# Kernel tuning notes

Hardware: AMD Instinct MI355X
Metric: run time of the kernel (lower is better)

The kernel has to match this reference:

```python
import jax, jax.numpy as jnp
import numpy as np

H = 1024      # hidden_dim == memory_dim (required by seq-axis concat)
M = 1024      # memory_dim
FF = 4096     # ff_dim
WIN = 16      # window_size
SLOTS = 10    # persistent memory slots
B, S = 2, 4096
EPS_LN = 1e-5
EPS_NORM = 1e-12


def _layernorm(x, g, b):
    m = jnp.mean(x, axis=-1, keepdims=True)
    v = jnp.var(x, axis=-1, keepdims=True)
    return (x - m) / jnp.sqrt(v + EPS_LN) * g + b


def setup_inputs() -> dict:
    key = jax.random.key(0)
    ks = jax.random.split(key, 12)

    def lin_w(k, out_d, in_d):
        return jax.random.normal(k, (out_d, in_d), jnp.float32) / np.sqrt(in_d)

    return {
        "x": jax.random.normal(ks[0], (B, S, H), jnp.float32),
        "mem_W": lin_w(ks[1], M, M), "mem_b": jnp.zeros((M,), jnp.float32),
        "P": jax.random.normal(ks[2], (SLOTS, M), jnp.float32),
        "Wi": lin_w(ks[3], M, H), "bi": jnp.zeros((M,), jnp.float32),
        "Wl1": lin_w(ks[4], M, M), "bl1": jnp.zeros((M,), jnp.float32),
        "Wl2": lin_w(ks[5], M, M), "bl2": jnp.zeros((M,), jnp.float32),
        "Wo": lin_w(ks[6], H, M), "bo": jnp.zeros((H,), jnp.float32),
        "fgate": jnp.ones((1,), jnp.float32),
        "lrate": jnp.ones((1,), jnp.float32),
        "Wg": lin_w(ks[7], H, 2 * H), "bg": jnp.zeros((H,), jnp.float32),
        "W1": lin_w(ks[8], FF, H), "b1": jnp.zeros((FF,), jnp.float32),
        "W2": lin_w(ks[9], H, FF), "b2": jnp.zeros((H,), jnp.float32),
        "g1": jnp.ones((H,), jnp.float32), "be1": jnp.zeros((H,), jnp.float32),
        "g2": jnp.ones((H,), jnp.float32), "be2": jnp.zeros((H,), jnp.float32),
        "g3": jnp.ones((H,), jnp.float32), "be3": jnp.zeros((H,), jnp.float32),
    }


def reference(x, mem_W, mem_b, P, Wi, bi, Wl1, bl1, Wl2, bl2, Wo, bo,
              fgate, lrate, Wg, bg, W1, b1, W2, b2,
              g1, be1, g2, be2, g3, be3):
    b, s, h = x.shape
    # k = concat(x, persistent) along seq; v = k.clone()
    k_full = jnp.concatenate([x, jnp.broadcast_to(P, (b,) + P.shape)], axis=1)  # [B, S+SLOTS, H]

    # sit at positions >= S and are never inside the window, so only x is attended.
    idx = jnp.arange(s)[:, None] + jnp.arange(-WIN, 1)[None, :]
    valid = idx >= 0
    k_win = k_full[:, jnp.maximum(idx, 0)]
    scores = jnp.einsum('bsh,bswh->bsw', x, k_win) * (h ** -0.5)
    scores = jnp.where(valid[None], scores, -jnp.inf)
    attn_out = jnp.einsum('bsw,bswh->bsh', jax.nn.softmax(scores, axis=-1), k_win)
    x1 = _layernorm(x + attn_out, g1, be1)

    # --- neural long-term memory (key == value since v = k.clone())
    kv = k_full.reshape(-1, h)
    kn = kv / jnp.maximum(jnp.linalg.norm(kv, axis=-1, keepdims=True), EPS_NORM)
    kp = kn @ Wi.T + bi          # projected key; value_proj is identical
    vp = kp
    hdd = jax.nn.silu(kp @ Wl1.T + bl1)
    hdd = jax.nn.silu(hdd @ Wl2.T + bl2)
    pred = hdd @ mem_W.T + mem_b
    diff = pred - vp
    n, m = diff.shape
    grad_W = (2.0 / (n * m)) * diff.T @ hdd          # d mse / d mem_W
    W_new = (1.0 - fgate) * mem_W + lrate * grad_W   # test-time memory update
    mem_out = hdd @ W_new.T + mem_b
    mo = (mem_out @ Wo.T + bo).reshape(b, -1, h)[:, :s]  # align with x seq length

    # --- gated fusion + FFN
    gate = jax.nn.sigmoid(jnp.concatenate([x1, mo], axis=-1) @ Wg.T + bg)
    combined = gate * x1 + (1.0 - gate) * mo
    x2 = _layernorm(x1 + combined, g2, be2)
    ff = jax.nn.silu(x2 @ W1.T + b1) @ W2.T + b2
    return _layernorm(x2 + ff, g3, be3)
```

## Files before the change

kernel.cpp:

```cpp
#include <hip/hip_runtime.h>
#include <hip/hip_bf16.h>

#define WIN 16
#define SLOTS 10
#define SS 4096
#define NTOK 8192
#define NKV 8212
#define NPOS 4106

typedef unsigned short u16;
typedef unsigned int u32;
typedef __attribute__((ext_vector_type(8))) short short8;
typedef __attribute__((ext_vector_type(4))) float f32x4;

__device__ __forceinline__ u16 f2bf(float f){
  union { float f; u32 u; } a; a.f = f;
  u32 r = (a.u + 0x7fff + ((a.u >> 16) & 1)) >> 16;
  return (u16)r;
}
__device__ __forceinline__ float bf2f(u16 v){
  union { u32 u; float f; } a; a.u = ((u32)v) << 16;
  return a.f;
}

#define GLOAD(gp, lp) __builtin_amdgcn_global_load_lds( \
    (const __attribute__((address_space(1))) void*)(gp), \
    (__attribute__((address_space(3))) void*)(lp), 16, 0, 0)

#define FENCE_BARRIER() do { \
    __builtin_amdgcn_sched_barrier(0); \
    __builtin_amdgcn_s_barrier(); \
    __builtin_amdgcn_sched_barrier(0); \
  } while(0)

__global__ __launch_bounds__(256) void cvt_bf16(const float4* __restrict__ in,
                                                ushort4* __restrict__ out, int n4){
  int i = blockIdx.x * 256 + threadIdx.x;
  if (i < n4){
    float4 v = in[i];
    ushort4 o; o.x=f2bf(v.x); o.y=f2bf(v.y); o.z=f2bf(v.z); o.w=f2bf(v.w);
    out[i] = o;
  }
}

__global__ __launch_bounds__(256) void attn_ln1(
    const float* __restrict__ x, const float* __restrict__ g1,
    const float* __restrict__ be1, u16* __restrict__ x1b)
{
  const int n = blockIdx.x;
  const int b = n >> 12, s = n & 4095;
  const int t = threadIdx.x, lane = t & 63, w = t >> 6;
  const float* xb = x + ((size_t)b << 22);
  const float4 q = ((const float4*)(xb + ((size_t)s << 10)))[t];
  const int j0 = (s >= WIN) ? 0 : (WIN - s);
  float kvv[17][4];
  float part[17];
  #pragma unroll
  for (int j=0;j<17;j++){
    float4 kk = make_float4(0.f,0.f,0.f,0.f);
    if (j >= j0) kk = ((const float4*)(xb + ((size_t)(s - WIN + j) << 10)))[t];
    kvv[j][0]=kk.x; kvv[j][1]=kk.y; kvv[j][2]=kk.z; kvv[j][3]=kk.w;
    part[j] = q.x*kk.x + q.y*kk.y + q.z*kk.z + q.w*kk.w;
  }
  __shared__ float red[17][4];
  #pragma unroll
  for (int j=0;j<17;j++){
    float v = part[j];
    #pragma unroll
    for (int off=32; off; off>>=1) v += __shfl_xor(v, off, 64);
    if (lane == 0) red[j][w] = v;
  }
  __syncthreads();
  __shared__ float wsh[17];
  if (t == 0){
    float sc[17];
    float mx = -3.0e38f;
    #pragma unroll
    for (int j=0;j<17;j++){
      float v = (red[j][0]+red[j][1]+red[j][2]+red[j][3]) * 0.03125f;
      sc[j] = v;
      if (j >= j0) mx = fmaxf(mx, v);
    }
    float ssum = 0.f;
    #pragma unroll
    for (int j=0;j<17;j++){
      float e = (j >= j0) ? expf(sc[j]-mx) : 0.f;
      wsh[j] = e; ssum += e;
    }
    float inv = 1.f/ssum;
    #pragma unroll
    for (int j=0;j<17;j++) wsh[j] *= inv;
  }
  __syncthreads();
  float y0=q.x, y1=q.y, y2=q.z, y3=q.w;
  #pragma unroll
  for (int j=0;j<17;j++){
    float wj = wsh[j];
    y0 += wj*kvv[j][0]; y1 += wj*kvv[j][1]; y2 += wj*kvv[j][2]; y3 += wj*kvv[j][3];
  }
  float s1 = y0+y1+y2+y3;
  float s2 = y0*y0+y1*y1+y2*y2+y3*y3;
  #pragma unroll
  for (int off=32; off; off>>=1){ s1 += __shfl_xor(s1, off, 64); s2 += __shfl_xor(s2, off, 64); }
  __shared__ float rsh[8];
  if (lane == 0){ rsh[w] = s1; rsh[4+w] = s2; }
  __syncthreads();
  float S1 = rsh[0]+rsh[1]+rsh[2]+rsh[3];
  float S2 = rsh[4]+rsh[5]+rsh[6]+rsh[7];
  float mean = S1 * (1.f/1024.f);
  float var  = S2 * (1.f/1024.f) - mean*mean;
  float rstd = 1.f/sqrtf(var + 1e-5f);
  float4 gv = ((const float4*)g1)[t];
  float4 bv = ((const float4*)be1)[t];
  ushort4 ob;
  ob.x = f2bf((y0-mean)*rstd*gv.x + bv.x);
  ob.y = f2bf((y1-mean)*rstd*gv.y + bv.y);
  ob.z = f2bf((y2-mean)*rstd*gv.z + bv.z);
  ob.w = f2bf((y3-mean)*rstd*gv.w + bv.w);
  ((ushort4*)x1b)[((size_t)n << 8) + t] = ob;
}

__global__ __launch_bounds__(256) void kv_norm(const float* __restrict__ x,
                                               const float* __restrict__ P,
                                               u16* __restrict__ kn)
{
  const int r = blockIdx.x;
  const int t = threadIdx.x, lane = t & 63, w = t >> 6;
  const int b = r / NPOS;
  const int pos = r - b*NPOS;
  const float* src = (pos < SS) ? (x + (((size_t)b*SS + pos) << 10))
                                : (P + ((size_t)(pos - SS) << 10));
  float4 v = ((const float4*)src)[t];
  float s2 = v.x*v.x + v.y*v.y + v.z*v.z + v.w*v.w;
  #pragma unroll
  for (int off=32; off; off>>=1) s2 += __shfl_xor(s2, off, 64);
  __shared__ float sh[4];
  if (lane == 0) sh[w] = s2;
  __syncthreads();
  float S = sh[0]+sh[1]+sh[2]+sh[3];
  float inv = 1.f / fmaxf(sqrtf(S), 1e-12f);
  ushort4 o; o.x=f2bf(v.x*inv); o.y=f2bf(v.y*inv); o.z=f2bf(v.z*inv); o.w=f2bf(v.w*inv);
  ((ushort4*)kn)[((size_t)r << 8) + t] = o;
}

template<int EPI, int SPLITA>
__global__ __launch_bounds__(256) void gemm_nt(
    const u16* __restrict__ A, const u16* __restrict__ A2,
    const u16* __restrict__ Bmat, const float* __restrict__ bias,
    const u16* __restrict__ auxb,
    float* __restrict__ Cf, u16* __restrict__ Cb,
    int N, int O, int ldA, int ldB, int klen)
{
  __shared__ __align__(16) u16 lA[2][128*64];
  __shared__ __align__(16) u16 lB[2][128*64];
  const int t = threadIdx.x;
  const int lane = t & 63;
  const int bm0 = blockIdx.x * 128;
  const int bn0 = blockIdx.y * 128;
  const int wid = t >> 6;
  const int wr = wid >> 1, wc = wid & 1;
  const int nkt = klen >> 6;

  f32x4 acc[4][4];
  #pragma unroll
  for (int i=0;i<4;i++)
    #pragma unroll
    for (int j=0;j<4;j++)
      acc[i][j] = (f32x4){0.f,0.f,0.f,0.f};

  const int srow = t >> 3;
  const int schunk = (((t & 7) ^ (srow & 7)) << 3);

  const u16* baseA[4]; const u16* baseA2[4]; const u16* baseB[4];
  #pragma unroll
  for (int i=0;i<4;i++){
    int gr = bm0 + srow + i*32; gr = gr < N ? gr : N-1;
    baseA[i] = A + (size_t)gr*(size_t)ldA + schunk;
    if (SPLITA) baseA2[i] = A2 + ((size_t)gr << 10) + schunk;
    int gb = bn0 + srow + i*32; gb = gb < O ? gb : O-1;
    baseB[i] = Bmat + (size_t)gb*(size_t)ldB + schunk;
  }

  auto stage = [&](int kt, int buf){
    const int kb = kt << 6;
    #pragma unroll
    for (int i=0;i<4;i++){
      const u16* src = SPLITA ? ((kb < 1024) ? baseA[i] + kb : baseA2[i] + (kb - 1024))
                              : baseA[i] + kb;
      GLOAD(src, &lA[buf][(i*256 + t) << 3]);
    }
    #pragma unroll
    for (int i=0;i<4;i++)
      GLOAD(baseB[i] + kb, &lB[buf][(i*256 + t) << 3]);
  };

  stage(0, 0);
  if (nkt > 1) stage(1, 1);

  const int l15 = lane & 15;
  const int rx = l15 & 7;
  const int cq = lane >> 4;

  for (int kt = 0; kt < nkt; ++kt){
    const int cur = kt & 1;
    if (kt + 1 < nkt) { asm volatile("s_waitcnt vmcnt(8)" ::: "memory"); }
    else              { asm volatile("s_waitcnt vmcnt(0)" ::: "memory"); }
    FENCE_BARRIER();
    #pragma unroll
    for (int kk=0;kk<2;kk++){
      const int soff = (((kk*4 + cq) ^ rx) << 3);
      short8 af[4], bfv[4];
      #pragma unroll
      for (int mi=0;mi<4;mi++)
        af[mi] = *(const short8*)(&lA[cur][((wr*64 + mi*16 + l15) << 6) + soff]);
      #pragma unroll
      for (int ni=0;ni<4;ni++)
        bfv[ni] = *(const short8*)(&lB[cur][((wc*64 + ni*16 + l15) << 6) + soff]);
      #pragma unroll
      for (int mi=0;mi<4;mi++)
        #pragma unroll
        for (int ni=0;ni<4;ni++)
          acc[mi][ni] = __builtin_amdgcn_mfma_f32_16x16x32_bf16(af[mi], bfv[ni], acc[mi][ni], 0, 0, 0);
    }
    FENCE_BARRIER();
    if (kt + 2 < nkt) stage(kt + 2, cur);
  }

  const int rbase = (lane >> 4) * 4;
  const int cidx = lane & 15;
  #pragma unroll
  for (int mi=0;mi<4;mi++){
    #pragma unroll
    for (int r=0;r<4;r++){
      const int n = bm0 + wr*64 + mi*16 + rbase + r;
      if (n >= N) continue;
      #pragma unroll
      for (int ni=0;ni<4;ni++){
        const int o = bn0 + wc*64 + ni*16 + cidx;
        float v = acc[mi][ni][r] + bias[o];
        if (EPI == 6){
          int b = n / NPOS;
          int pos = n - b*NPOS;
          if (pos < SS){
            Cb[(((size_t)(b*SS + pos)) << 10) + o] = f2bf(v);
          }
        } else {
          size_t idx = (size_t)n*(size_t)O + o;
          if (EPI == 0){ Cf[idx] = v; }
          else if (EPI == 1){ float sv = v/(1.f+__expf(-v)); Cb[idx] = f2bf(sv); }
          else if (EPI == 2){ Cb[idx] = f2bf(v); }
          else if (EPI == 4){ Cb[idx] = f2bf(v - bf2f(auxb[idx])); }
          else if (EPI == 5){ Cb[idx] = f2bf(1.f/(1.f+__expf(-v))); }
        }
      }
    }
  }
}

template<int EPI>
__global__ __launch_bounds__(512, 2) void gemm_256(
    const u16* __restrict__ A, const u16* __restrict__ Bmat,
    const float* __restrict__ bias,
    float* __restrict__ Cf, u16* __restrict__ Cb,
    int N, int O, int ldA, int ldB, int klen)
{
  __shared__ __align__(16) u16 lA[2][256*64];
  __shared__ __align__(16) u16 lB[2][256*64];
  const int t = threadIdx.x;
  const int lane = t & 63;
  const int wid = t >> 6;
  const int wr = wid >> 2, wc = wid & 3;
  const int bm0 = blockIdx.x * 256;
  const int bn0 = blockIdx.y * 256;
  const int nkt = klen >> 6;

  f32x4 acc[8][4];
  #pragma unroll
  for (int i=0;i<8;i++)
    #pragma unroll
    for (int j=0;j<4;j++)
      acc[i][j] = (f32x4){0.f,0.f,0.f,0.f};

  const int srow = t >> 3;
  const int schunk = (((t & 7) ^ (srow & 7)) << 3);

  const u16* baseA[4]; const u16* baseB[4];
  #pragma unroll
  for (int i=0;i<4;i++){
    int gr = bm0 + srow + i*64; gr = gr < N ? gr : N-1;
    baseA[i] = A + (size_t)gr*(size_t)ldA + schunk;
    int gb = bn0 + srow + i*64; gb = gb < O ? gb : O-1;
    baseB[i] = Bmat + (size_t)gb*(size_t)ldB + schunk;
  }

  auto stage = [&](int kt, int buf){
    const int kb = kt << 6;
    #pragma unroll
    for (int i=0;i<4;i++)
      GLOAD(baseA[i] + kb, &lA[buf][(i*512 + t) << 3]);
    #pragma unroll
    for (int i=0;i<4;i++)
      GLOAD(baseB[i] + kb, &lB[buf][(i*512 + t) << 3]);
  };

  stage(0, 0);
  if (nkt > 1) stage(1, 1);

  const int l15 = lane & 15;
  const int rx = l15 & 7;
  const int cq = lane >> 4;

  for (int kt = 0; kt < nkt; ++kt){
    const int cur = kt & 1;
    if (kt + 1 < nkt) { asm volatile("s_waitcnt vmcnt(8)" ::: "memory"); }
    else              { asm volatile("s_waitcnt vmcnt(0)" ::: "memory"); }
    FENCE_BARRIER();
    #pragma unroll
    for (int kk=0;kk<2;kk++){
      const int soff = (((kk*4 + cq) ^ rx) << 3);
      short8 af[8], bfv[4];
      #pragma unroll
      for (int ni=0;ni<4;ni++)
        bfv[ni] = *(const short8*)(&lB[cur][((wc*64 + ni*16 + l15) << 6) + soff]);
      #pragma unroll
      for (int mi=0;mi<8;mi++)
        af[mi] = *(const short8*)(&lA[cur][((wr*128 + mi*16 + l15) << 6) + soff]);
      #pragma unroll
      for (int mi=0;mi<8;mi++)
        #pragma unroll
        for (int ni=0;ni<4;ni++)
          acc[mi][ni] = __builtin_amdgcn_mfma_f32_16x16x32_bf16(af[mi], bfv[ni], acc[mi][ni], 0, 0, 0);
    }
    FENCE_BARRIER();
    if (kt + 2 < nkt) stage(kt + 2, cur);
  }

  const int rbase = (lane >> 4) * 4;
  const int cidx = lane & 15;
  #pragma unroll
  for (int mi=0;mi<8;mi++){
    #pragma unroll
    for (int r=0;r<4;r++){
      const int n = bm0 + wr*128 + mi*16 + rbase + r;
      if (n >= N) continue;
      #pragma unroll
      for (int ni=0;ni<4;ni++){
        const int o = bn0 + wc*64 + ni*16 + cidx;
        float v = acc[mi][ni][r] + bias[o];
        size_t idx = (size_t)n*(size_t)O + o;
        if (EPI == 0){ Cf[idx] = v; }
        else if (EPI == 1){ float sv = v/(1.f+__expf(-v)); Cb[idx] = f2bf(sv); }
        else if (EPI == 2){ Cb[idx] = f2bf(v); }
      }
    }
  }
}

#define NSPLIT 6
__global__ __launch_bounds__(256) void gemm_tn(
    const u16* __restrict__ A, const u16* __restrict__ B,
    float* __restrict__ part0, float* __restrict__ part1)
{
  __shared__ __align__(16) u16 lA[128*64];
  __shared__ __align__(16) u16 lB[128*64];
  const int t = threadIdx.x, lane = t & 63;
  const int i0 = blockIdx.x * 128, j0 = blockIdx.y * 128, z = blockIdx.z;
  const int wid = t >> 6, wr = wid >> 1, wc = wid & 1;
  const int TILES = (NKV + 63) >> 6;
  const int PER = (TILES + NSPLIT - 1) / NSPLIT;
  const int kt0 = z * PER;
  const int ktend = (kt0 + PER < TILES) ? (kt0 + PER) : TILES;

  f32x4 acc[4][4];
  #pragma unroll
  for (int i=0;i<4;i++)
    #pragma unroll
    for (int j=0;j<4;j++)
      acc[i][j] = (f32x4){0.f,0.f,0.f,0.f};

  const int p = t & 31;
  const int g = t >> 5;

  auto loadr = [&](int kt, short8 R[8]){
    const int n0 = kt << 6;
    const int na = n0 + 2*p, nb = na + 1;
    short8 z8 = (short8){0,0,0,0,0,0,0,0};
    R[0]=z8;R[1]=z8;R[2]=z8;R[3]=z8;R[4]=z8;R[5]=z8;R[6]=z8;R[7]=z8;
    if (na < NKV){
      const u16* ra = A + (size_t)na*1024 + i0 + g*16;
      R[0] = *(const short8*)ra; R[1] = *(const short8*)(ra+8);
      const u16* rb = B + (size_t)na*1024 + j0 + g*16;
      R[4] = *(const short8*)rb; R[5] = *(const short8*)(rb+8);
    }
    if (nb < NKV){
      const u16* ra = A + (size_t)nb*1024 + i0 + g*16;
      R[2] = *(const short8*)ra; R[3] = *(const short8*)(ra+8);
      const u16* rb = B + (size_t)nb*1024 + j0 + g*16;
      R[6] = *(const short8*)rb; R[7] = *(const short8*)(rb+8);
    }
  };

  short8 cr[8], nr[8];
  loadr(kt0, cr);

  const int pc = p >> 2, pl = p & 3;

  for (int kt = kt0; kt < ktend; ++kt){
    if (kt + 1 < ktend) loadr(kt + 1, nr);
    asm volatile("" ::: "memory");
    FENCE_BARRIER();
    u32* wA = (u32*)lA; u32* wB = (u32*)lB;
    #pragma unroll
    for (int e=0;e<8;e++){
      const int s = (pc ^ e) * 4 + pl;
      wA[(g*16 + e)*32 + s]     = ((u32)(u16)cr[0][e]) | (((u32)(u16)cr[2][e]) << 16);
      wB[(g*16 + e)*32 + s]     = ((u32)(u16)cr[4][e]) | (((u32)(u16)cr[6][e]) << 16);
    }
    #pragma unroll
    for (int e=0;e<8;e++){
      const int s = (pc ^ e) * 4 + pl;
      wA[(g*16 + 8 + e)*32 + s] = ((u32)(u16)cr[1][e]) | (((u32)(u16)cr[3][e]) << 16);
      wB[(g*16 + 8 + e)*32 + s] = ((u32)(u16)cr[5][e]) | (((u32)(u16)cr[7][e]) << 16);
    }
    asm volatile("s_waitcnt lgkmcnt(0)" ::: "memory");
    FENCE_BARRIER();
    const int l15 = lane & 15;
    const int rx = l15 & 7;
    const int cq = lane >> 4;
    #pragma unroll
    for (int kk=0;kk<2;kk++){
      const int soff = (((kk*4 + cq) ^ rx) << 3);
      short8 af[4], bfv[4];
      #pragma unroll
      for (int mi=0;mi<4;mi++)
        af[mi] = *(const short8*)(lA + ((wr*64 + mi*16 + l15) << 6) + soff);
      #pragma unroll
      for (int ni=0;ni<4;ni++)
        bfv[ni] = *(const short8*)(lB + ((wc*64 + ni*16 + l15) << 6) + soff);
      #pragma unroll
      for (int mi=0;mi<4;mi++)
        #pragma unroll
        for (int ni=0;ni<4;ni++)
          acc[mi][ni] = __builtin_amdgcn_mfma_f32_16x16x32_bf16(af[mi], bfv[ni], acc[mi][ni], 0, 0, 0);
    }
    #pragma unroll
    for (int e=0;e<8;e++) cr[e] = nr[e];
  }

  float* dst = (z < 4) ? (part0 + ((size_t)z << 20)) : (part1 + ((size_t)(z-4) << 20));
  const int rbase = (lane >> 4) * 4;
  const int cidx = lane & 15;
  #pragma unroll
  for (int mi=0;mi<4;mi++)
    #pragma unroll
    for (int r=0;r<4;r++){
      const int i = i0 + wr*64 + mi*16 + rbase + r;
      #pragma unroll
      for (int ni=0;ni<4;ni++){
        const int j = j0 + wc*64 + ni*16 + cidx;
        dst[((size_t)i << 10) + j] = acc[mi][ni][r];
      }
    }
}

__global__ __launch_bounds__(256) void wnew_k(const float* __restrict__ part0,
                                              const float* __restrict__ part1,
                                              const float* __restrict__ memW,
                                              const float* __restrict__ fg,
                                              const float* __restrict__ lr,
                                              u16* __restrict__ out)
{
  int i = blockIdx.x*256 + threadIdx.x;
  float s = part0[i] + part0[i + (1<<20)] + part0[i + (2<<20)] + part0[i + (3<<20)]
          + part1[i] + part1[i + (1<<20)];
  const float scale = 2.f / ((float)NKV * 1024.f);
  float v = (1.f - fg[0])*memW[i] + lr[0]*scale*s;
  out[i] = f2bf(v);
}

__global__ __launch_bounds__(256) void ln_gate(
    const u16* __restrict__ x1b, const u16* __restrict__ gateb,
    const u16* __restrict__ mob, const float* __restrict__ g2,
    const float* __restrict__ be2, u16* __restrict__ x2b)
{
  const int n = blockIdx.x;
  const int t = threadIdx.x, lane = t & 63, w = t >> 6;
  const size_t rb = (size_t)n << 8;
  ushort4 xa = ((const ushort4*)x1b)[rb+t];
  ushort4 ga = ((const ushort4*)gateb)[rb+t];
  ushort4 ma = ((const ushort4*)mob)[rb+t];
  float a0=bf2f(xa.x),a1=bf2f(xa.y),a2=bf2f(xa.z),a3=bf2f(xa.w);
  float g0=bf2f(ga.x),g1v=bf2f(ga.y),g2v=bf2f(ga.z),g3v=bf2f(ga.w);
  float m0=bf2f(ma.x),m1=bf2f(ma.y),m2=bf2f(ma.z),m3=bf2f(ma.w);
  float y0 = a0 + g0*a0 + (1.f-g0)*m0;
  float y1 = a1 + g1v*a1 + (1.f-g1v)*m1;
  float y2 = a2 + g2v*a2 + (1.f-g2v)*m2;
  float y3 = a3 + g3v*a3 + (1.f-g3v)*m3;
  float s1 = y0+y1+y2+y3;
  float s2 = y0*y0+y1*y1+y2*y2+y3*y3;
  #pragma unroll
  for (int off=32; off; off>>=1){ s1 += __shfl_xor(s1, off, 64); s2 += __shfl_xor(s2, off, 64); }
  __shared__ float rsh[8];
  if (lane == 0){ rsh[w] = s1; rsh[4+w] = s2; }
  __syncthreads();
  float S1 = rsh[0]+rsh[1]+rsh[2]+rsh[3];
  float S2 = rsh[4]+rsh[5]+rsh[6]+rsh[7];
  float mean = S1 * (1.f/1024.f);
  float var  = S2 * (1.f/1024.f) - mean*mean;
  float rstd = 1.f/sqrtf(var + 1e-5f);
  float4 gv = ((const float4*)g2)[t];
  float4 bv = ((const float4*)be2)[t];
  ushort4 ob;
  ob.x = f2bf((y0-mean)*rstd*gv.x + bv.x);
  ob.y = f2bf((y1-mean)*rstd*gv.y + bv.y);
  ob.z = f2bf((y2-mean)*rstd*gv.z + bv.z);
  ob.w = f2bf((y3-mean)*rstd*gv.w + bv.w);
  ((ushort4*)x2b)[rb + t] = ob;
}

__global__ __launch_bounds__(256) void ln_final(
    const u16* __restrict__ x2b, const float* __restrict__ g3,
    const float* __restrict__ be3, float* __restrict__ out)
{
  const int n = blockIdx.x;
  const int t = threadIdx.x, lane = t & 63, w = t >> 6;
  const size_t rb = (size_t)n << 8;
  ushort4 xa = ((const ushort4*)x2b)[rb+t];
  float4 f = ((const float4*)out)[rb+t];
  float y0 = bf2f(xa.x)+f.x, y1 = bf2f(xa.y)+f.y, y2 = bf2f(xa.z)+f.z, y3 = bf2f(xa.w)+f.w;
  float s1 = y0+y1+y2+y3;
  float s2 = y0*y0+y1*y1+y2*y2+y3*y3;
  #pragma unroll
  for (int off=32; off; off>>=1){ s1 += __shfl_xor(s1, off, 64); s2 += __shfl_xor(s2, off, 64); }
  __shared__ float rsh[8];
  if (lane == 0){ rsh[w] = s1; rsh[4+w] = s2; }
  __syncthreads();
  float S1 = rsh[0]+rsh[1]+rsh[2]+rsh[3];
  float S2 = rsh[4]+rsh[5]+rsh[6]+rsh[7];
  float mean = S1 * (1.f/1024.f);
  float var  = S2 * (1.f/1024.f) - mean*mean;
  float rstd = 1.f/sqrtf(var + 1e-5f);
  float4 gv = ((const float4*)g3)[t];
  float4 bv = ((const float4*)be3)[t];
  float4 o;
  o.x = (y0-mean)*rstd*gv.x + bv.x;
  o.y = (y1-mean)*rstd*gv.y + bv.y;
  o.z = (y2-mean)*rstd*gv.z + bv.z;
  o.w = (y3-mean)*rstd*gv.w + bv.w;
  ((float4*)out)[rb + t] = o;
}

extern "C" void kernel_launch(void* const* d_in, const int* in_sizes, int n_in,
                              void* d_out, int out_size, void* d_ws, size_t ws_size,
                              hipStream_t stream)
{
  const float* x    = (const float*)d_in[0];
  const float* memW = (const float*)d_in[1];
  const float* memb = (const float*)d_in[2];
  const float* P    = (const float*)d_in[3];
  const float* Wi   = (const float*)d_in[4];
  const float* bi   = (const float*)d_in[5];
  const float* Wl1  = (const float*)d_in[6];
  const float* bl1  = (const float*)d_in[7];
  const float* Wl2  = (const float*)d_in[8];
  const float* bl2  = (const float*)d_in[9];
  const float* Wo   = (const float*)d_in[10];
  const float* bo   = (const float*)d_in[11];
  const float* fg   = (const float*)d_in[12];
  const float* lr   = (const float*)d_in[13];
  const float* Wg   = (const float*)d_in[14];
  const float* bg   = (const float*)d_in[15];
  const float* W1   = (const float*)d_in[16];
  const float* b1   = (const float*)d_in[17];
  const float* W2   = (const float*)d_in[18];
  const float* b2   = (const float*)d_in[19];
  const float* g1   = (const float*)d_in[20];
  const float* be1  = (const float*)d_in[21];
  const float* g2   = (const float*)d_in[22];
  const float* be2  = (const float*)d_in[23];
  const float* g3   = (const float*)d_in[24];
  const float* be3  = (const float*)d_in[25];
  float* out = (float*)d_out;

  const size_t SZ_TOK = (size_t)NTOK*1024*2;
  const size_t SZ_KV  = (size_t)NKV*1024*2;
  char* base = (char*)d_ws;
  size_t off = 0;
  auto alloc = [&](size_t bytes) -> char* {
    char* p = base + off;
    off += (bytes + 255) & ~(size_t)255;
    return p;
  };
  u16* x1b   = (u16*)alloc(SZ_TOK);
  u16* knb   = (u16*)alloc(SZ_KV);
  u16* h1b   = (u16*)alloc(SZ_KV);
  u16* hddb  = (u16*)alloc(SZ_KV);
  u16* kpb   = (u16*)alloc(SZ_KV);
  u16* wnewb = (u16*)alloc((size_t)1024*1024*2);
  u16* WiB   = (u16*)alloc((size_t)1024*1024*2);
  u16* Wl1B  = (u16*)alloc((size_t)1024*1024*2);
  u16* Wl2B  = (u16*)alloc((size_t)1024*1024*2);
  u16* memWB = (u16*)alloc((size_t)1024*1024*2);
  u16* WoB   = (u16*)alloc((size_t)1024*1024*2);
  u16* WgB   = (u16*)alloc((size_t)1024*2048*2);
  u16* W1B   = (u16*)alloc((size_t)4096*1024*2);
  u16* W2B   = (u16*)alloc((size_t)1024*4096*2);
  if (ws_size < off) return;

  u16*   diffb   = knb;
  float* part0   = (float*)kpb;
  float* part1   = (float*)WiB;
  u16*   memoutb = knb;
  u16*   mob     = h1b;
  u16*   gateb   = hddb;
  u16*   x2b     = kpb;
  u16*   ff1b    = x1b;

  auto cvt = [&](const float* src, u16* dst, int nelem){
    cvt_bf16<<<nelem/1024, 256, 0, stream>>>((const float4*)src, (ushort4*)dst, nelem/4);
  };
  cvt(Wi,   WiB,   1024*1024);
  cvt(Wl1,  Wl1B,  1024*1024);
  cvt(Wl2,  Wl2B,  1024*1024);
  cvt(memW, memWB, 1024*1024);
  cvt(Wo,   WoB,   1024*1024);
  cvt(Wg,   WgB,   1024*2048);
  cvt(W1,   W1B,   4096*1024);
  cvt(W2,   W2B,   1024*4096);

  attn_ln1<<<NTOK, 256, 0, stream>>>(x, g1, be1, x1b);
  kv_norm <<<NKV,  256, 0, stream>>>(x, P, knb);

  dim3 gkv(65, 8, 1);
  gemm_nt<2,0><<<gkv, 256, 0, stream>>>(knb, nullptr, WiB, bi, nullptr, nullptr, kpb, NKV, 1024, 1024, 1024, 1024);
  gemm_nt<1,0><<<gkv, 256, 0, stream>>>(kpb, nullptr, Wl1B, bl1, nullptr, nullptr, h1b, NKV, 1024, 1024, 1024, 1024);
  gemm_nt<1,0><<<gkv, 256, 0, stream>>>(h1b, nullptr, Wl2B, bl2, nullptr, nullptr, hddb, NKV, 1024, 1024, 1024, 1024);
  gemm_nt<4,0><<<gkv, 256, 0, stream>>>(hddb, nullptr, memWB, memb, kpb, nullptr, diffb, NKV, 1024, 1024, 1024, 1024);
  gemm_tn<<<dim3(8, 8, NSPLIT), 256, 0, stream>>>(diffb, hddb, part0, part1);
  wnew_k<<<4096, 256, 0, stream>>>(part0, part1, memW, fg, lr, wnewb);
  gemm_nt<2,0><<<gkv, 256, 0, stream>>>(hddb, nullptr, wnewb, memb, nullptr, nullptr, memoutb, NKV, 1024, 1024, 1024, 1024);
  gemm_nt<6,0><<<gkv, 256, 0, stream>>>(memoutb, nullptr, WoB, bo, nullptr, nullptr, mob, NKV, 1024, 1024, 1024, 1024);
  gemm_nt<5,1><<<dim3(64, 8, 1), 256, 0, stream>>>(x1b, mob, WgB, bg, nullptr, nullptr, gateb, NTOK, 1024, 1024, 2048, 2048);
  ln_gate<<<NTOK, 256, 0, stream>>>(x1b, gateb, mob, g2, be2, x2b);
  gemm_256<1><<<dim3(32, 16, 1), 512, 0, stream>>>(x2b, W1B, b1, nullptr, ff1b, NTOK, 4096, 1024, 1024, 1024);
  gemm_nt<0,0><<<dim3(64, 8, 1), 256, 0, stream>>>(ff1b, nullptr, W2B, b2, nullptr, out, nullptr, NTOK, 1024, 4096, 4096, 4096);
  ln_final<<<NTOK, 256, 0, stream>>>(x2b, g3, be3, out);
}
```

Before: 649.6 us.

## Deepen gemm_256 pipeline to four half-K stages and merge weight conversions

The 256x256 FFN GEMM now stages K in 32-wide halves across four LDS buffers with a three-deep prefetch. A and B loads are interleaved between two MFMA half-phases, and s_setprio brackets the MFMA blocks. The goal is to hide global-load latency better while keeping the same LDS footprint. The eight weight conversion launches are also merged into one kernel to cut launch overhead. The new swizzle and waitcnt accounting must stay consistent, and the finer-grained stages add more barriers.

```diff
diff --git a/kernel.cpp b/kernel.cpp
--- a/kernel.cpp
+++ b/kernel.cpp
@@ -33,14 +33,29 @@
     __builtin_amdgcn_sched_barrier(0); \
   } while(0)
 
-__global__ __launch_bounds__(256) void cvt_bf16(const float4* __restrict__ in,
-                                                ushort4* __restrict__ out, int n4){
+__global__ __launch_bounds__(256) void cvt_all(
+    const float4* __restrict__ s0, const float4* __restrict__ s1,
+    const float4* __restrict__ s2, const float4* __restrict__ s3,
+    const float4* __restrict__ s4, const float4* __restrict__ s5,
+    const float4* __restrict__ s6, const float4* __restrict__ s7,
+    ushort4* __restrict__ d0, ushort4* __restrict__ d1,
+    ushort4* __restrict__ d2, ushort4* __restrict__ d3,
+    ushort4* __restrict__ d4, ushort4* __restrict__ d5,
+    ushort4* __restrict__ d6, ushort4* __restrict__ d7)
+{
   int i = blockIdx.x * 256 + threadIdx.x;
-  if (i < n4){
-    float4 v = in[i];
-    ushort4 o; o.x=f2bf(v.x); o.y=f2bf(v.y); o.z=f2bf(v.z); o.w=f2bf(v.w);
-    out[i] = o;
-  }
+  const float4* s; ushort4* d; int base;
+  if      (i <  262144){ s=s0; d=d0; base=0; }
+  else if (i <  524288){ s=s1; d=d1; base=262144; }
+  else if (i <  786432){ s=s2; d=d2; base=524288; }
+  else if (i < 1048576){ s=s3; d=d3; base=786432; }
+  else if (i < 1310720){ s=s4; d=d4; base=1048576; }
+  else if (i < 1835008){ s=s5; d=d5; base=1310720; }
+  else if (i < 2883584){ s=s6; d=d6; base=1835008; }
+  else                 { s=s7; d=d7; base=2883584; }
+  float4 v = s[i - base];
+  ushort4 o; o.x=f2bf(v.x); o.y=f2bf(v.y); o.z=f2bf(v.z); o.w=f2bf(v.w);
+  d[i - base] = o;
 }
 
 __global__ __launch_bounds__(256) void attn_ln1(
@@ -264,15 +279,15 @@
     float* __restrict__ Cf, u16* __restrict__ Cb,
     int N, int O, int ldA, int ldB, int klen)
 {
-  __shared__ __align__(16) u16 lA[2][256*64];
-  __shared__ __align__(16) u16 lB[2][256*64];
+  __shared__ __align__(16) u16 lA[4][256*32];
+  __shared__ __align__(16) u16 lB[4][256*32];
   const int t = threadIdx.x;
   const int lane = t & 63;
   const int wid = t >> 6;
   const int wr = wid >> 2, wc = wid & 3;
   const int bm0 = blockIdx.x * 256;
   const int bn0 = blockIdx.y * 256;
-  const int nkt = klen >> 6;
+  const int nkh = (klen >> 6) * 2;
 
   f32x4 acc[8][4];
   #pragma unroll
@@ -281,58 +296,79 @@
     for (int j=0;j<4;j++)
       acc[i][j] = (f32x4){0.f,0.f,0.f,0.f};
 
-  const int srow = t >> 3;
-  const int schunk = (((t & 7) ^ (srow & 7)) << 3);
-
-  const u16* baseA[4]; const u16* baseB[4];
-  #pragma unroll
-  for (int i=0;i<4;i++){
-    int gr = bm0 + srow + i*64; gr = gr < N ? gr : N-1;
-    baseA[i] = A + (size_t)gr*(size_t)ldA + schunk;
-    int gb = bn0 + srow + i*64; gb = gb < O ? gb : O-1;
-    baseB[i] = Bmat + (size_t)gb*(size_t)ldB + schunk;
-  }
-
-  auto stage = [&](int kt, int buf){
-    const int kb = kt << 6;
-    #pragma unroll
-    for (int i=0;i<4;i++)
-      GLOAD(baseA[i] + kb, &lA[buf][(i*512 + t) << 3]);
-    #pragma unroll
-    for (int i=0;i<4;i++)
-      GLOAD(baseB[i] + kb, &lB[buf][(i*512 + t) << 3]);
+  const int srow = t >> 2;
+  const int sch  = t & 3;
+  const int csw  = ((sch ^ ((srow >> 1) & 3)) << 3);
+  int gr0 = bm0 + srow;       gr0 = gr0 < N ? gr0 : N-1;
+  int gr1 = bm0 + srow + 128; gr1 = gr1 < N ? gr1 : N-1;
+  int gb0 = bn0 + srow;       gb0 = gb0 < O ? gb0 : O-1;
+  int gb1 = bn0 + srow + 128; gb1 = gb1 < O ? gb1 : O-1;
+  const u16* baseA0 = A    + (size_t)gr0*(size_t)ldA + csw;
+  const u16* baseA1 = A    + (size_t)gr1*(size_t)ldA + csw;
+  const u16* baseB0 = Bmat + (size_t)gb0*(size_t)ldB + csw;
+  const u16* baseB1 = Bmat + (size_t)gb1*(size_t)ldB + csw;
+  const int ldsLo = srow*32 + (sch << 3);
+  const int ldsHi = (srow + 128)*32 + (sch << 3);
+
+  auto stageA = [&](int j){
+    const int kb = j << 5;
+    const int s = j & 3;
+    GLOAD(baseA0 + kb, &lA[s][ldsLo]);
+    GLOAD(baseA1 + kb, &lA[s][ldsHi]);
   };
-
-  stage(0, 0);
-  if (nkt > 1) stage(1, 1);
+  auto stageB = [&](int j){
+    const int kb = j << 5;
+    const int s = j & 3;
+    GLOAD(baseB0 + kb, &lB[s][ldsLo]);
+    GLOAD(baseB1 + kb, &lB[s][ldsHi]);
+  };
+
+  stageA(0); stageB(0);
+  if (nkh > 1){ stageA(1); stageB(1); }
+  if (nkh > 2){ stageA(2); stageB(2); }
 
   const int l15 = lane & 15;
-  const int rx = l15 & 7;
-  const int cq = lane >> 4;
-
-  for (int kt = 0; kt < nkt; ++kt){
-    const int cur = kt & 1;
-    if (kt + 1 < nkt) { asm volatile("s_waitcnt vmcnt(8)" ::: "memory"); }
-    else              { asm volatile("s_waitcnt vmcnt(0)" ::: "memory"); }
+  const int cq  = lane >> 4;
+  const int chS = ((cq ^ ((l15 >> 1) & 3)) << 3);
+
+  for (int j = 0; j < nkh; ++j){
+    const int s = j & 3;
+    const int rem = nkh - 1 - j;
+    if (rem >= 2)      { asm volatile("s_waitcnt vmcnt(8)" ::: "memory"); }
+    else if (rem == 1) { asm volatile("s_waitcnt vmcnt(4)" ::: "memory"); }
+    else               { asm volatile("s_waitcnt vmcnt(0)" ::: "memory"); }
     FENCE_BARRIER();
-    #pragma unroll
-    for (int kk=0;kk<2;kk++){
-      const int soff = (((kk*4 + cq) ^ rx) << 3);
-      short8 af[8], bfv[4];
+    short8 af[4], bfv[4];
+    #pragma unroll
+    for (int ni=0;ni<4;ni++)
+      bfv[ni] = *(const short8*)(&lB[s][((wc*64 + ni*16 + l15) * 32) + chS]);
+    #pragma unroll
+    for (int mi=0;mi<4;mi++)
+      af[mi] = *(const short8*)(&lA[s][((wr*128 + mi*16 + l15) * 32) + chS]);
+    if (j + 3 < nkh) stageA(j + 3);
+    __builtin_amdgcn_sched_barrier(0);
+    __builtin_amdgcn_s_setprio(1);
+    #pragma unroll
+    for (int mi=0;mi<4;mi++)
       #pragma unroll
       for (int ni=0;ni<4;ni++)
-        bfv[ni] = *(const short8*)(&lB[cur][((wc*64 + ni*16 + l15) << 6) + soff]);
-      #pragma unroll
-      for (int mi=0;mi<8;mi++)
-        af[mi] = *(const short8*)(&lA[cur][((wr*128 + mi*16 + l15) << 6) + soff]);
-      #pragma unroll
-      for (int mi=0;mi<8;mi++)
-        #pragma unroll
-        for (int ni=0;ni<4;ni++)
-          acc[mi][ni] = __builtin_amdgcn_mfma_f32_16x16x32_bf16(af[mi], bfv[ni], acc[mi][ni], 0, 0, 0);
-    }
+        acc[mi][ni] = __builtin_amdgcn_mfma_f32_16x16x32_bf16(af[mi], bfv[ni], acc[mi][ni], 0, 0, 0);
+    __builtin_amdgcn_s_setprio(0);
+    __builtin_amdgcn_sched_barrier(0);
     FENCE_BARRIER();
-    if (kt + 2 < nkt) stage(kt + 2, cur);
+    #pragma unroll
+    for (int mi=0;mi<4;mi++)
+      af[mi] = *(const short8*)(&lA[s][((wr*128 + (mi+4)*16 + l15) * 32) + chS]);
+    if (j + 3 < nkh) stageB(j + 3);
+    __builtin_amdgcn_sched_barrier(0);
+    __builtin_amdgcn_s_setprio(1);
+    #pragma unroll
+    for (int mi=0;mi<4;mi++)
+      #pragma unroll
+      for (int ni=0;ni<4;ni++)
+        acc[mi+4][ni] = __builtin_amdgcn_mfma_f32_16x16x32_bf16(af[mi], bfv[ni], acc[mi+4][ni], 0, 0, 0);
+    __builtin_amdgcn_s_setprio(0);
+    __builtin_amdgcn_sched_barrier(0);
   }
 
   const int rbase = (lane >> 4) * 4;
@@ -616,17 +652,11 @@
   u16*   x2b     = kpb;
   u16*   ff1b    = x1b;
 
-  auto cvt = [&](const float* src, u16* dst, int nelem){
-    cvt_bf16<<<nelem/1024, 256, 0, stream>>>((const float4*)src, (ushort4*)dst, nelem/4);
-  };
-  cvt(Wi,   WiB,   1024*1024);
-  cvt(Wl1,  Wl1B,  1024*1024);
-  cvt(Wl2,  Wl2B,  1024*1024);
-  cvt(memW, memWB, 1024*1024);
-  cvt(Wo,   WoB,   1024*1024);
-  cvt(Wg,   WgB,   1024*2048);
-  cvt(W1,   W1B,   4096*1024);
-  cvt(W2,   W2B,   1024*4096);
+  cvt_all<<<15360, 256, 0, stream>>>(
+      (const float4*)Wi, (const float4*)Wl1, (const float4*)Wl2, (const float4*)memW,
+      (const float4*)Wo, (const float4*)Wg, (const float4*)W1, (const float4*)W2,
+      (ushort4*)WiB, (ushort4*)Wl1B, (ushort4*)Wl2B, (ushort4*)memWB,
+      (ushort4*)WoB, (ushort4*)WgB, (ushort4*)W1B, (ushort4*)W2B);
 
   attn_ln1<<<NTOK, 256, 0, stream>>>(x, g1, be1, x1b);
   kv_norm <<<NKV,  256, 0, stream>>>(x, P, knb);
```

Result: faster. 633.7 us (-2.5%).
